# Kernel optimization log

Measured on AMD Instinct MI355X. Metric: run time of the kernel, lower is better.

The kernel has to match this reference:

```python
import jax, jax.numpy as jnp
import numpy as np

IN_FEATURES = 64
OUT_FEATURES = 16
GRID_SIZE = 8
SPLINE_ORDER = 3
GRID_MIN, GRID_MAX = -1.0, 1.0
N = 100000


def make_grid():
    # grid = arange(-spline_order, grid_size+spline_order+1) * m + grid_min, expanded per input feature
    m = (GRID_MAX - GRID_MIN) / GRID_SIZE
    g = jnp.arange(-SPLINE_ORDER, GRID_SIZE + SPLINE_ORDER + 1, dtype=jnp.float32) * m + GRID_MIN
    return jnp.broadcast_to(g, (IN_FEATURES, g.shape[0]))  # [in, gs+2*so+1]


def setup_inputs() -> dict:
    key = jax.random.key(0)
    k1, k2 = jax.random.split(key)
    # x must lie inside the grid range [-1, 1]
    x = jax.random.uniform(k1, (N, IN_FEATURES), dtype=jnp.float32, minval=-1.0, maxval=1.0)
    y = jax.random.normal(k2, (N, IN_FEATURES, OUT_FEATURES), dtype=jnp.float32)
    grid = make_grid()
    return {"x": x, "y": y, "grid": grid}


def bspline_basis(x, grid):
    """Cox-de Boor recursion. x: [N, in], grid: [in, G]. Returns [N, in, gs+so]."""
    xe = x[..., None]  # [N, in, 1]
    # order-0 indicator basis
    b = ((xe >= grid[:, :-1]) & (xe < grid[:, 1:])).astype(x.dtype)  # [N, in, G-1]
    for k in range(1, SPLINE_ORDER + 1):
        left = (xe - grid[:, : -(k + 1)]) / (grid[:, k:-1] - grid[:, : -(k + 1)])
        right = (grid[:, k + 1:] - xe) / (grid[:, k + 1:] - grid[:, 1:-k])
        b = left * b[..., :-1] + right * b[..., 1:]
    return b  # [N, in, gs+so]


def reference(x, y, grid):
    # curve(): least-squares fit of spline-basis coefficients, batched over input features.
    k = bspline_basis(x, grid)            # [N, in, K]
    A = jnp.transpose(k, (1, 0, 2))        # [in, N, K]
    B = jnp.transpose(y, (1, 0, 2))        # [in, N, out]
    # full-rank least squares via normal equations (equivalent to torch.linalg.lstsq solution)
    AtA = jnp.einsum('ink,inl->ikl', A, A)  # [in, K, K]
    AtB = jnp.einsum('ink,ino->iko', A, B)  # [in, K, out]
    X = jnp.linalg.solve(AtA, AtB)          # [in, K, out]
    return jnp.transpose(X, (2, 0, 1))      # [out, in, K]
```

## Files before the change

kernel.cpp:

```cpp
#include <hip/hip_runtime.h>

#define N_ROWS 100000
#define IN_F 64
#define OUT_F 16
#define KB 11
#define SLOTS 216
#define PB (IN_F * SLOTS)
#define CHUNK_ROWS 16
#define NCHUNKS (N_ROWS / CHUNK_ROWS)
#define RGROUPS 16
#define MAX_NB 512

__global__ __launch_bounds__(256) void kan_partial(const float* __restrict__ x,
                                                   const float* __restrict__ y,
                                                   float* __restrict__ ws) {
    __shared__ float k_lds[CHUNK_ROWS * IN_F * 12];
    const int tid = threadIdx.x;
    const int i4  = tid >> 2;
    const int q   = tid & 3;
    const int o4  = q * 4;

    float4 atb[KB];
    float  atA[KB];
#pragma unroll
    for (int kk = 0; kk < KB; ++kk) {
        atb[kk] = make_float4(0.f, 0.f, 0.f, 0.f);
        atA[kk] = 0.f;
    }

    for (int ch = blockIdx.x; ch < NCHUNKS; ch += gridDim.x) {
        const int n0 = ch * CHUNK_ROWS;
#pragma unroll
        for (int s = 0; s < 4; ++s) {
            const int pp = tid + s * 256;
            const float xv = x[n0 * IN_F + pp];
            float tpos = (xv + 1.0f) * 4.0f;
            int c = (int)floorf(tpos);
            c = c < 0 ? 0 : (c > 7 ? 7 : c);
            const float u   = tpos - (float)c;
            const float omu = 1.0f - u;
            const float b0 = omu * omu * omu * (1.0f / 6.0f);
            const float b3 = u * u * u * (1.0f / 6.0f);
            const float b1 = (0.5f * u - 1.0f) * u * u + (2.0f / 3.0f);
            const float b2 = 1.0f - b0 - b1 - b3;
            float* kp = &k_lds[pp * 12];
            const float4 z = make_float4(0.f, 0.f, 0.f, 0.f);
            ((float4*)kp)[0] = z; ((float4*)kp)[1] = z; ((float4*)kp)[2] = z;
            kp[c] = b0; kp[c + 1] = b1; kp[c + 2] = b2; kp[c + 3] = b3;
        }
        __syncthreads();

        const size_t ybase = (size_t)n0 * (IN_F * OUT_F) + (size_t)i4 * OUT_F + o4;
#pragma unroll 4
        for (int r = 0; r < CHUNK_ROWS; ++r) {
            const float* kp = &k_lds[(r * IN_F + i4) * 12];
            const float4 k0 = ((const float4*)kp)[0];
            const float4 k1 = ((const float4*)kp)[1];
            const float4 k2 = ((const float4*)kp)[2];
            const float k[12] = {k0.x, k0.y, k0.z, k0.w, k1.x, k1.y, k1.z, k1.w,
                                 k2.x, k2.y, k2.z, k2.w};
            const float4 y4 = *(const float4*)(y + ybase + (size_t)r * (IN_F * OUT_F));
#pragma unroll
            for (int kk = 0; kk < KB; ++kk) {
                atb[kk].x += k[kk] * y4.x;
                atb[kk].y += k[kk] * y4.y;
                atb[kk].z += k[kk] * y4.z;
                atb[kk].w += k[kk] * y4.w;
            }
            if (q == 0) {
#pragma unroll
                for (int a = 0; a < 11; ++a) atA[a] += k[a] * k[a];
            } else if (q == 1) {
#pragma unroll
                for (int a = 0; a < 10; ++a) atA[a] += k[a] * k[a + 1];
            } else if (q == 2) {
#pragma unroll
                for (int a = 0; a < 9; ++a) atA[a] += k[a] * k[a + 2];
            } else {
#pragma unroll
                for (int a = 0; a < 8; ++a) atA[a] += k[a] * k[a + 3];
            }
        }
        __syncthreads();
    }

    float* base = ws + ((size_t)blockIdx.x * IN_F + i4) * SLOTS;
    const int bandBase = (q == 0) ? 0 : (q == 1) ? 11 : (q == 2) ? 21 : 30;
    const int bandCnt  = 11 - q;
    for (int m = 0; m < bandCnt; ++m) base[bandBase + m] = atA[m];
#pragma unroll
    for (int kk = 0; kk < KB; ++kk)
        *(float4*)(base + 40 + kk * 16 + o4) = atb[kk];
}

__global__ __launch_bounds__(256) void kan_reduce(float* __restrict__ ws, int nb) {
    const int gid = blockIdx.x * 256 + threadIdx.x;
    const int e = gid % PB;
    const int g = gid / PB;
    float val = 0.f;
#pragma unroll 4
    for (int p = g; p < nb; p += RGROUPS) val += ws[(size_t)p * PB + e];
    ws[((size_t)nb + g) * PB + e] = val;
}

__global__ __launch_bounds__(320) void kan_solve(const float* __restrict__ ws2,
                                                 float* __restrict__ out) {
    __shared__ float M[11][28];
    const int i = blockIdx.x;
    const int tid = threadIdx.x;

    float val = 0.f;
    if (tid < SLOTS) {
#pragma unroll
        for (int g = 0; g < RGROUPS; ++g)
            val += ws2[(size_t)g * PB + (size_t)i * SLOTS + tid];
    }
    {
        const int r = tid / 28, c = tid % 28;
        if (r < 11) M[r][c] = 0.f;
    }
    __syncthreads();
    if (tid < 38) {
        int d, a;
        if (tid < 11)      { d = 0; a = tid; }
        else if (tid < 21) { d = 1; a = tid - 11; }
        else if (tid < 30) { d = 2; a = tid - 21; }
        else               { d = 3; a = tid - 30; }
        M[a][a + d] = val;
        M[a + d][a] = val;
    } else if (tid >= 40 && tid < SLOTS) {
        const int e = tid - 40;
        M[e >> 4][11 + (e & 15)] = val;
    }
    __syncthreads();

    const int rr = tid / 28, cc = tid % 28;
    const bool active = (rr < 11) && (cc < 27);
    for (int p = 0; p < 11; ++p) {
        float pd = 1.f, mpc = 0.f, mrp = 0.f, mrc = 0.f;
        if (active) { pd = M[p][p]; mpc = M[p][cc]; mrp = M[rr][p]; mrc = M[rr][cc]; }
        __syncthreads();
        if (active) {
            const float s = mpc / pd;
            M[rr][cc] = (rr == p) ? s : mrc - mrp * s;
        }
        __syncthreads();
    }

    if (tid < 176) {
        const int o = tid / 11, r2 = tid % 11;
        out[o * (IN_F * KB) + i * KB + r2] = M[r2][11 + o];
    }
}

extern "C" void kernel_launch(void* const* d_in, const int* in_sizes, int n_in,
                              void* d_out, int out_size, void* d_ws, size_t ws_size,
                              hipStream_t stream) {
    const float* x = (const float*)d_in[0];
    const float* y = (const float*)d_in[1];
    float* out = (float*)d_out;
    float* ws  = (float*)d_ws;

    const size_t per_block = (size_t)PB * sizeof(float);
    long cap = (long)(ws_size / per_block) - RGROUPS;
    int nb = (int)(cap < 1 ? 1 : (cap > MAX_NB ? MAX_NB : cap));
    if (nb > NCHUNKS) nb = NCHUNKS;

    kan_partial<<<nb, 256, 0, stream>>>(x, y, ws);
    kan_reduce<<<(RGROUPS * PB) / 256, 256, 0, stream>>>(ws, nb);
    kan_solve<<<IN_F, 320, 0, stream>>>(ws + (size_t)nb * PB, out);
}
```

Before: 560.9 us.

## Stream contiguous row ranges per block with register prefetch and no block barriers

Each block now owns a contiguous range of rows instead of striding over 16-row chunks. For each row it prefetches the next row's x and y into registers. The basis values are computed per feature by one lane into a small LDS slot and read by the other three lanes of the same wavefront, which removes the __syncthreads pairs. The block cap rises to 1024 and launch bounds request 4 blocks per SM, to get more waves in flight on the bandwidth-bound partial sums. The catch is that the LDS handoff relies on ordering within a wavefront with no barrier, and each row is still processed serially with only one row of prefetch.

New measurement: 579.3 us. 3.3% more time.

```diff
diff --git a/kernel.cpp b/kernel.cpp
--- a/kernel.cpp
+++ b/kernel.cpp
@@ -6,19 +6,18 @@
 #define KB 11
 #define SLOTS 216
 #define PB (IN_F * SLOTS)
-#define CHUNK_ROWS 16
-#define NCHUNKS (N_ROWS / CHUNK_ROWS)
 #define RGROUPS 16
-#define MAX_NB 512
+#define MAX_NB 1024
 
-__global__ __launch_bounds__(256) void kan_partial(const float* __restrict__ x,
-                                                   const float* __restrict__ y,
-                                                   float* __restrict__ ws) {
-    __shared__ float k_lds[CHUNK_ROWS * IN_F * 12];
+__global__ __launch_bounds__(256, 4) void kan_partial(const float* __restrict__ x,
+                                                      const float* __restrict__ y,
+                                                      float* __restrict__ ws, int nb) {
+    __shared__ float kd[IN_F * 12];
     const int tid = threadIdx.x;
-    const int i4  = tid >> 2;
-    const int q   = tid & 3;
-    const int o4  = q * 4;
+    const int f = tid >> 2;
+    const int q = tid & 3;
+    const int o4 = q * 4;
+    float* slot = &kd[f * 12];
 
     float4 atb[KB];
     float  atA[KB];
@@ -28,38 +27,41 @@
         atA[kk] = 0.f;
     }
 
-    for (int ch = blockIdx.x; ch < NCHUNKS; ch += gridDim.x) {
-        const int n0 = ch * CHUNK_ROWS;
-#pragma unroll
-        for (int s = 0; s < 4; ++s) {
-            const int pp = tid + s * 256;
-            const float xv = x[n0 * IN_F + pp];
-            float tpos = (xv + 1.0f) * 4.0f;
-            int c = (int)floorf(tpos);
-            c = c < 0 ? 0 : (c > 7 ? 7 : c);
-            const float u   = tpos - (float)c;
-            const float omu = 1.0f - u;
-            const float b0 = omu * omu * omu * (1.0f / 6.0f);
-            const float b3 = u * u * u * (1.0f / 6.0f);
-            const float b1 = (0.5f * u - 1.0f) * u * u + (2.0f / 3.0f);
-            const float b2 = 1.0f - b0 - b1 - b3;
-            float* kp = &k_lds[pp * 12];
-            const float4 z = make_float4(0.f, 0.f, 0.f, 0.f);
-            ((float4*)kp)[0] = z; ((float4*)kp)[1] = z; ((float4*)kp)[2] = z;
-            kp[c] = b0; kp[c + 1] = b1; kp[c + 2] = b2; kp[c + 3] = b3;
-        }
-        __syncthreads();
+    const int per = (N_ROWS + nb - 1) / nb;
+    const int lo = blockIdx.x * per;
+    const int hi = (lo + per < N_ROWS) ? (lo + per) : N_ROWS;
 
-        const size_t ybase = (size_t)n0 * (IN_F * OUT_F) + (size_t)i4 * OUT_F + o4;
-#pragma unroll 4
-        for (int r = 0; r < CHUNK_ROWS; ++r) {
-            const float* kp = &k_lds[(r * IN_F + i4) * 12];
-            const float4 k0 = ((const float4*)kp)[0];
-            const float4 k1 = ((const float4*)kp)[1];
-            const float4 k2 = ((const float4*)kp)[2];
+    if (lo < hi) {
+        float xv = 0.f;
+        if (q == 0) xv = x[(size_t)lo * IN_F + f];
+        float4 y4 = *(const float4*)(y + (size_t)lo * (IN_F * OUT_F) + tid * 4);
+
+        for (int n = lo; n < hi; ++n) {
+            const int np = (n + 1 < hi) ? (n + 1) : n;
+            float xnext = 0.f;
+            if (q == 0) xnext = x[(size_t)np * IN_F + f];
+            const float4 ynext = *(const float4*)(y + (size_t)np * (IN_F * OUT_F) + tid * 4);
+
+            if (q == 0) {
+                const float tpos = (xv + 1.0f) * 4.0f;
+                int c = (int)tpos;
+                c = c < 0 ? 0 : (c > 7 ? 7 : c);
+                const float u = tpos - (float)c;
+                const float omu = 1.0f - u;
+                const float b0 = omu * omu * omu * (1.0f / 6.0f);
+                const float b3 = u * u * u * (1.0f / 6.0f);
+                const float b1 = (0.5f * u - 1.0f) * u * u + (2.0f / 3.0f);
+                const float b2 = 1.0f - b0 - b1 - b3;
+                const float4 z = make_float4(0.f, 0.f, 0.f, 0.f);
+                ((float4*)slot)[0] = z; ((float4*)slot)[1] = z; ((float4*)slot)[2] = z;
+                slot[c] = b0; slot[c + 1] = b1; slot[c + 2] = b2; slot[c + 3] = b3;
+            }
+            const float4 k0 = ((const float4*)slot)[0];
+            const float4 k1 = ((const float4*)slot)[1];
+            const float4 k2 = ((const float4*)slot)[2];
             const float k[12] = {k0.x, k0.y, k0.z, k0.w, k1.x, k1.y, k1.z, k1.w,
                                  k2.x, k2.y, k2.z, k2.w};
-            const float4 y4 = *(const float4*)(y + ybase + (size_t)r * (IN_F * OUT_F));
+
 #pragma unroll
             for (int kk = 0; kk < KB; ++kk) {
                 atb[kk].x += k[kk] * y4.x;
@@ -80,13 +82,14 @@
 #pragma unroll
                 for (int a = 0; a < 8; ++a) atA[a] += k[a] * k[a + 3];
             }
+            xv = xnext;
+            y4 = ynext;
         }
-        __syncthreads();
     }
 
-    float* base = ws + ((size_t)blockIdx.x * IN_F + i4) * SLOTS;
+    float* base = ws + ((size_t)blockIdx.x * IN_F + f) * SLOTS;
     const int bandBase = (q == 0) ? 0 : (q == 1) ? 11 : (q == 2) ? 21 : 30;
-    const int bandCnt  = 11 - q;
+    const int bandCnt = 11 - q;
     for (int m = 0; m < bandCnt; ++m) base[bandBase + m] = atA[m];
 #pragma unroll
     for (int kk = 0; kk < KB; ++kk)
@@ -164,9 +167,8 @@
     const size_t per_block = (size_t)PB * sizeof(float);
     long cap = (long)(ws_size / per_block) - RGROUPS;
     int nb = (int)(cap < 1 ? 1 : (cap > MAX_NB ? MAX_NB : cap));
-    if (nb > NCHUNKS) nb = NCHUNKS;
 
-    kan_partial<<<nb, 256, 0, stream>>>(x, y, ws);
+    kan_partial<<<nb, 256, 0, stream>>>(x, y, ws, nb);
     kan_reduce<<<(RGROUPS * PB) / 256, 256, 0, stream>>>(ws, nb);
     kan_solve<<<IN_F, 320, 0, stream>>>(ws + (size_t)nb * PB, out);
 }
```
